# Performance work log

Measured on AMD Instinct MI355X. Metric: run time of the kernel, lower is better.

Reference implementation:

```python
import jax, jax.numpy as jnp
import numpy as np

GRID_MIN, GRID_MAX, GRID_SIZE = -4.0, 4.0, 12
BANDWIDTH = (GRID_MAX - GRID_MIN) / max(GRID_SIZE - 1, 1)  # 8/11


def setup_inputs() -> dict:
    key = jax.random.key(0)
    k1, k2, k3, k4 = jax.random.split(key, 4)
    B, I, O, G = 16384, 512, 512, GRID_SIZE
    x = jax.random.normal(k1, (B, I), dtype=jnp.float32)
    coeff = jax.random.normal(k2, (I, O, G), dtype=jnp.float32) * 0.05
    base_w = jax.random.normal(k3, (O, I), dtype=jnp.float32) * (1.0 / np.sqrt(I))
    base_b = jax.random.normal(k4, (O,), dtype=jnp.float32) * 0.01
    centers = jnp.linspace(GRID_MIN, GRID_MAX, G, dtype=jnp.float32)
    return {"x": x, "coeff": coeff, "base_w": base_w, "base_b": base_b, "centers": centers}


def reference(x, coeff, base_w, base_b, centers):
    # RBF basis: [B, I, G]
    diff = (x[..., None] - centers) / jnp.float32(BANDWIDTH)
    basis = jnp.exp(-0.5 * diff * diff)
    # spline contraction over in_dim and grid: [B, O]
    spline = jnp.einsum('big,iog->bo', basis, coeff)
    # residual base linear (torch Linear: x @ W^T + b)
    return spline + x @ base_w.T + base_b
```

## Files before the change

kernel.cpp:

```cpp
#include <hip/hip_runtime.h>
#include <hip/hip_bf16.h>


#define M_DIM 16384
#define N_DIM 512
#define I_DIM 512
#define KTOT  6656
#define NSTEP 104

typedef short short8 __attribute__((ext_vector_type(8)));
typedef float f32x16 __attribute__((ext_vector_type(16)));
typedef unsigned int u32x4 __attribute__((ext_vector_type(4)));

#define CVTPK(dst, lo, hi) \
  asm("v_cvt_pk_bf16_f32 %0, %1, %2" : "=v"(dst) : "v"(lo), "v"(hi))

__device__ __forceinline__ unsigned short f2bf(float f) {
  union { float f; unsigned int u; } c; c.f = f;
  unsigned int r = (c.u + 0x7FFFu + ((c.u >> 16) & 1)) >> 16;
  return (unsigned short)r;
}

__global__ __launch_bounds__(256) void prep_w(const float* __restrict__ coeff,
                                              const float* __restrict__ base_w,
                                              unsigned short* __restrict__ Wb2) {
  int t = blockIdx.x * 256 + threadIdx.x;
  int e0 = (t & 1) * 4;
  int go = t >> 1;
  int o  = go & 511;
  int g  = go >> 9;
  int k4 = g * 8 + e0;
  int ic = k4 / 832;
  int rem = k4 - ic * 832;
  int slot = rem >> 6;
  int ii = rem & 63;
  int i = ic * 64 + ii;
  float v0, v1, v2, v3;
  if (slot == 0) {
    const float4 bw = *(const float4*)(base_w + (size_t)o * I_DIM + i);
    v0 = bw.x; v1 = bw.y; v2 = bw.z; v3 = bw.w;
  } else {
    int gg = slot - 1;
    const float* cp = coeff + (size_t)i * (N_DIM * 12) + o * 12 + gg;
    v0 = cp[0]; v1 = cp[6144]; v2 = cp[2 * 6144]; v3 = cp[3 * 6144];
  }
  ushort4 s;
  s.x = f2bf(v0); s.y = f2bf(v1); s.z = f2bf(v2); s.w = f2bf(v3);
  *(ushort4*)(Wb2 + (size_t)go * 8 + e0) = s;
}

__global__ __launch_bounds__(512, 2) void kan_gemm(const float* __restrict__ x,
                                                   const unsigned short* __restrict__ Wb2,
                                                   const float* __restrict__ bias,
                                                   float* __restrict__ out) {
  __shared__ unsigned short Asw[2][8 * 128 * 8];
  __shared__ unsigned short Bsw[2][8 * 256 * 8];

  const int tid  = threadIdx.x;
  const int lane = tid & 63;
  const int wid  = tid >> 6;
  const int wm   = wid >> 2, wn = wid & 3;

  const int rb = blockIdx.x >> 1;
  const int cb = blockIdx.x & 1;
  const int M0 = rb * 128;
  const int N0 = cb * 256;

  const int arow = tid & 127;
  const int kgp  = tid >> 7;
  const float* xg = x + (size_t)(M0 + arow) * I_DIM + kgp * 16;
  const int aoff0 = ((kgp * 2) * 128 + arow) * 16;
  const int aoff1 = ((kgp * 2 + 1) * 128 + arow) * 16;

  const unsigned short* bsrc[4];
  int bdst[4];
#pragma unroll
  for (int q = 0; q < 4; ++q) {
    bsrc[q] = Wb2 + ((size_t)wid * 512 + N0 + q * 64 + lane) * 8;
    bdst[q] = (wid * 256 + q * 64) * 16;
  }

  const int l31 = lane & 31;
  const int aBase = ((lane >> 5) * 128 + wm * 64 + l31) * 16;
  const int bBase = ((lane >> 5) * 256 + wn * 64 + l31) * 16;

  f32x16 acc[2][2];
#pragma unroll
  for (int i = 0; i < 2; ++i)
#pragma unroll
    for (int j = 0; j < 2; ++j)
#pragma unroll
      for (int r = 0; r < 16; ++r) acc[i][j][r] = 0.f;

  float4 xq[4];
#pragma unroll
  for (int q = 0; q < 4; ++q) xq[q] = *(const float4*)(xg + q * 4);
  float bb[16], ff[16];
  int gslot = 0, gic = 0;

  auto emitA = [&](char* pA) {
    unsigned int w[8];
    if (gslot == 0) {
      float f[16];
#pragma unroll
      for (int q = 0; q < 4; ++q) {
        f[q*4+0] = xq[q].x; f[q*4+1] = xq[q].y; f[q*4+2] = xq[q].z; f[q*4+3] = xq[q].w;
      }
#pragma unroll
      for (int j = 0; j < 8; ++j) CVTPK(w[j], f[2*j], f[2*j+1]);
      *(u32x4*)(pA + aoff0) = (u32x4){w[0], w[1], w[2], w[3]};
      *(u32x4*)(pA + aoff1) = (u32x4){w[4], w[5], w[6], w[7]};
#pragma unroll
      for (int j = 0; j < 16; ++j) {
        float u = fmaf(f[j], 1.375f, 5.5f);
        bb[j] = exp2f(-0.72134752044448170f * u * u);
        ff[j] = exp2f(fmaf(u, 1.44269504088896340f, -0.72134752044448170f));
      }
      if (gic < 7) {
        const float* xn = xg + (gic + 1) * 64;
#pragma unroll
        for (int q = 0; q < 4; ++q) xq[q] = *(const float4*)(xn + q * 4);
        ++gic;
      }
    } else {
#pragma unroll
      for (int j = 0; j < 8; ++j) CVTPK(w[j], bb[2*j], bb[2*j+1]);
      *(u32x4*)(pA + aoff0) = (u32x4){w[0], w[1], w[2], w[3]};
      *(u32x4*)(pA + aoff1) = (u32x4){w[4], w[5], w[6], w[7]};
#pragma unroll
      for (int j = 0; j < 16; ++j) {
        bb[j] *= ff[j];
        ff[j] *= 0.36787944117144233f;
      }
    }
    gslot = (gslot == 12) ? 0 : gslot + 1;
  };

  emitA((char*)&Asw[0][0]);
#pragma unroll
  for (int q = 0; q < 4; ++q)
    __builtin_amdgcn_global_load_lds(
        (const __attribute__((address_space(1))) void*)(bsrc[q]),
        (__attribute__((address_space(3))) void*)((char*)&Bsw[0][0] + bdst[q]), 16, 0, 0);
  __syncthreads();

  int buf = 0;
  for (int ks = 0; ks < NSTEP; ++ks) {
    const int nxt = buf ^ 1;
    if (ks < NSTEP - 1) {
      const size_t ko = (size_t)(ks + 1) * 32768;
#pragma unroll
      for (int q = 0; q < 4; ++q)
        __builtin_amdgcn_global_load_lds(
            (const __attribute__((address_space(1))) void*)(bsrc[q] + ko),
            (__attribute__((address_space(3))) void*)((char*)&Bsw[nxt][0] + bdst[q]), 16, 0, 0);
      emitA((char*)&Asw[nxt][0]);
    }
    const char* pA = (const char*)&Asw[buf][0];
    const char* pB = (const char*)&Bsw[buf][0];
#pragma unroll
    for (int s = 0; s < 4; ++s) {
      const char* a = pA + aBase + s * 4096;
      const char* b = pB + bBase + s * 8192;
      short8 a0 = *(const short8*)(a);
      short8 a1 = *(const short8*)(a + 512);
      short8 b0 = *(const short8*)(b);
      short8 b1 = *(const short8*)(b + 512);
      acc[0][0] = __builtin_amdgcn_mfma_f32_32x32x16_bf16(a0, b0, acc[0][0], 0, 0, 0);
      acc[0][1] = __builtin_amdgcn_mfma_f32_32x32x16_bf16(a0, b1, acc[0][1], 0, 0, 0);
      acc[1][0] = __builtin_amdgcn_mfma_f32_32x32x16_bf16(a1, b0, acc[1][0], 0, 0, 0);
      acc[1][1] = __builtin_amdgcn_mfma_f32_32x32x16_bf16(a1, b1, acc[1][1], 0, 0, 0);
    }
    __syncthreads();
    buf = nxt;
  }

  float bv[2];
#pragma unroll
  for (int fn = 0; fn < 2; ++fn) bv[fn] = bias[N0 + wn * 64 + fn * 32 + l31];
  const int rbase = (lane >> 5) * 4;
#pragma unroll
  for (int fm = 0; fm < 2; ++fm) {
#pragma unroll
    for (int fn = 0; fn < 2; ++fn) {
      const size_t cix = (size_t)(N0 + wn * 64 + fn * 32 + l31);
#pragma unroll
      for (int r = 0; r < 16; ++r) {
        int row = M0 + wm * 64 + fm * 32 + (r & 3) + 8 * (r >> 2) + rbase;
        out[(size_t)row * N_DIM + cix] = acc[fm][fn][r] + bv[fn];
      }
    }
  }
}

extern "C" void kernel_launch(void* const* d_in, const int* in_sizes, int n_in,
                              void* d_out, int out_size, void* d_ws, size_t ws_size,
                              hipStream_t stream) {
  const float* x      = (const float*)d_in[0];
  const float* coeff  = (const float*)d_in[1];
  const float* base_w = (const float*)d_in[2];
  const float* base_b = (const float*)d_in[3];
  unsigned short* Wb2 = (unsigned short*)d_ws;

  prep_w<<<3328, 256, 0, stream>>>(coeff, base_w, Wb2);
  kan_gemm<<<256, 512, 0, stream>>>(x, Wb2, base_b, (float*)d_out);
}
```

Baseline: 138.0 us.

## Triple-buffer B tiles with prefetch distance two and manual waitcnt barriers

Grows the B shared-memory buffer from two to three stages and issues global-to-LDS loads two steps ahead. The full __syncthreads is replaced by explicit s_waitcnt vmcnt counts, so later loads can stay in flight across the barrier. It also raises wave priority around the MFMA block. This hides global load latency better, but uses more LDS, which may affect 2-blocks-per-CU occupancy, and the hand-tuned vmcnt counts are fragile.

```diff
diff --git a/kernel.cpp b/kernel.cpp
--- a/kernel.cpp
+++ b/kernel.cpp
@@ -54,7 +54,7 @@
                                                    const float* __restrict__ bias,
                                                    float* __restrict__ out) {
   __shared__ unsigned short Asw[2][8 * 128 * 8];
-  __shared__ unsigned short Bsw[2][8 * 256 * 8];
+  __shared__ unsigned short Bsw[3][8 * 256 * 8];
 
   const int tid  = threadIdx.x;
   const int lane = tid & 63;
@@ -96,83 +96,138 @@
 #pragma unroll
   for (int q = 0; q < 4; ++q) xq[q] = *(const float4*)(xg + q * 4);
   float bb[16], ff[16];
-  int gslot = 0, gic = 0;
-
-  auto emitA = [&](char* pA) {
-    unsigned int w[8];
-    if (gslot == 0) {
-      float f[16];
-#pragma unroll
-      for (int q = 0; q < 4; ++q) {
-        f[q*4+0] = xq[q].x; f[q*4+1] = xq[q].y; f[q*4+2] = xq[q].z; f[q*4+3] = xq[q].w;
-      }
-#pragma unroll
-      for (int j = 0; j < 8; ++j) CVTPK(w[j], f[2*j], f[2*j+1]);
-      *(u32x4*)(pA + aoff0) = (u32x4){w[0], w[1], w[2], w[3]};
-      *(u32x4*)(pA + aoff1) = (u32x4){w[4], w[5], w[6], w[7]};
-#pragma unroll
-      for (int j = 0; j < 16; ++j) {
-        float u = fmaf(f[j], 1.375f, 5.5f);
-        bb[j] = exp2f(-0.72134752044448170f * u * u);
-        ff[j] = exp2f(fmaf(u, 1.44269504088896340f, -0.72134752044448170f));
-      }
-      if (gic < 7) {
-        const float* xn = xg + (gic + 1) * 64;
-#pragma unroll
-        for (int q = 0; q < 4; ++q) xq[q] = *(const float4*)(xn + q * 4);
-        ++gic;
-      }
-    } else {
-#pragma unroll
-      for (int j = 0; j < 8; ++j) CVTPK(w[j], bb[2*j], bb[2*j+1]);
-      *(u32x4*)(pA + aoff0) = (u32x4){w[0], w[1], w[2], w[3]};
-      *(u32x4*)(pA + aoff1) = (u32x4){w[4], w[5], w[6], w[7]};
-#pragma unroll
-      for (int j = 0; j < 16; ++j) {
-        bb[j] *= ff[j];
-        ff[j] *= 0.36787944117144233f;
-      }
-    }
-    gslot = (gslot == 12) ? 0 : gslot + 1;
-  };
-
-  emitA((char*)&Asw[0][0]);
+  int gic = 0;
+
+  float f0[16];
+#pragma unroll
+  for (int q = 0; q < 4; ++q) {
+    f0[q*4+0] = xq[q].x; f0[q*4+1] = xq[q].y; f0[q*4+2] = xq[q].z; f0[q*4+3] = xq[q].w;
+  }
+#pragma unroll
+  for (int q = 0; q < 4; ++q) xq[q] = *(const float4*)(xg + 64 + q * 4);
+  gic = 1;
 #pragma unroll
   for (int q = 0; q < 4; ++q)
     __builtin_amdgcn_global_load_lds(
         (const __attribute__((address_space(1))) void*)(bsrc[q]),
         (__attribute__((address_space(3))) void*)((char*)&Bsw[0][0] + bdst[q]), 16, 0, 0);
-  __syncthreads();
-
-  int buf = 0;
-  for (int ks = 0; ks < NSTEP; ++ks) {
-    const int nxt = buf ^ 1;
-    if (ks < NSTEP - 1) {
-      const size_t ko = (size_t)(ks + 1) * 32768;
+#pragma unroll
+  for (int q = 0; q < 4; ++q)
+    __builtin_amdgcn_global_load_lds(
+        (const __attribute__((address_space(1))) void*)(bsrc[q] + 32768),
+        (__attribute__((address_space(3))) void*)((char*)&Bsw[1][0] + bdst[q]), 16, 0, 0);
+  {
+    unsigned int w[8];
+#pragma unroll
+    for (int j = 0; j < 8; ++j) CVTPK(w[j], f0[2*j], f0[2*j+1]);
+    char* pA = (char*)&Asw[0][0];
+    *(u32x4*)(pA + aoff0) = (u32x4){w[0], w[1], w[2], w[3]};
+    *(u32x4*)(pA + aoff1) = (u32x4){w[4], w[5], w[6], w[7]};
+#pragma unroll
+    for (int j = 0; j < 16; ++j) {
+      float u = fmaf(f0[j], 1.375f, 5.5f);
+      bb[j] = exp2f(-0.72134752044448170f * u * u);
+      ff[j] = exp2f(fmaf(u, 1.44269504088896340f, -0.72134752044448170f));
+    }
+  }
+  __builtin_amdgcn_sched_barrier(0);
+  asm volatile("s_waitcnt vmcnt(4) lgkmcnt(0)" ::: "memory");
+  __builtin_amdgcn_sched_barrier(0);
+  __builtin_amdgcn_s_barrier();
+  __builtin_amdgcn_sched_barrier(0);
+
+  int nslot = 1;
+  int cur3  = 0;
+  for (int t = 0; t < NSTEP; ++t) {
+    const bool emit = (t < NSTEP - 1);
+    const bool s0   = (nslot == 0);
+    bool reload = false;
+    float f[16];
+
+    if (emit && s0) {
+#pragma unroll
+      for (int q = 0; q < 4; ++q) {
+        f[q*4+0] = xq[q].x; f[q*4+1] = xq[q].y; f[q*4+2] = xq[q].z; f[q*4+3] = xq[q].w;
+      }
+      if (gic < 7) {
+        const float* xn = xg + (size_t)(gic + 1) * 64;
+#pragma unroll
+        for (int q = 0; q < 4; ++q) xq[q] = *(const float4*)(xn + q * 4);
+        reload = true;
+      }
+      ++gic;
+    }
+
+    if (t < NSTEP - 2) {
+      const int nx3 = (cur3 >= 1) ? cur3 - 1 : 2;
+      char* bb2 = (char*)&Bsw[nx3][0];
+      const size_t ko = (size_t)(t + 2) * 32768;
 #pragma unroll
       for (int q = 0; q < 4; ++q)
         __builtin_amdgcn_global_load_lds(
             (const __attribute__((address_space(1))) void*)(bsrc[q] + ko),
-            (__attribute__((address_space(3))) void*)((char*)&Bsw[nxt][0] + bdst[q]), 16, 0, 0);
-      emitA((char*)&Asw[nxt][0]);
-    }
-    const char* pA = (const char*)&Asw[buf][0];
-    const char* pB = (const char*)&Bsw[buf][0];
-#pragma unroll
-    for (int s = 0; s < 4; ++s) {
-      const char* a = pA + aBase + s * 4096;
-      const char* b = pB + bBase + s * 8192;
-      short8 a0 = *(const short8*)(a);
-      short8 a1 = *(const short8*)(a + 512);
-      short8 b0 = *(const short8*)(b);
-      short8 b1 = *(const short8*)(b + 512);
-      acc[0][0] = __builtin_amdgcn_mfma_f32_32x32x16_bf16(a0, b0, acc[0][0], 0, 0, 0);
-      acc[0][1] = __builtin_amdgcn_mfma_f32_32x32x16_bf16(a0, b1, acc[0][1], 0, 0, 0);
-      acc[1][0] = __builtin_amdgcn_mfma_f32_32x32x16_bf16(a1, b0, acc[1][0], 0, 0, 0);
-      acc[1][1] = __builtin_amdgcn_mfma_f32_32x32x16_bf16(a1, b1, acc[1][1], 0, 0, 0);
-    }
-    __syncthreads();
-    buf = nxt;
+            (__attribute__((address_space(3))) void*)(bb2 + bdst[q]), 16, 0, 0);
+    }
+
+    if (emit) {
+      char* pA = (char*)&Asw[(t + 1) & 1][0];
+      unsigned int w[8];
+      if (s0) {
+#pragma unroll
+        for (int j = 0; j < 8; ++j) CVTPK(w[j], f[2*j], f[2*j+1]);
+        *(u32x4*)(pA + aoff0) = (u32x4){w[0], w[1], w[2], w[3]};
+        *(u32x4*)(pA + aoff1) = (u32x4){w[4], w[5], w[6], w[7]};
+#pragma unroll
+        for (int j = 0; j < 16; ++j) {
+          float u = fmaf(f[j], 1.375f, 5.5f);
+          bb[j] = exp2f(-0.72134752044448170f * u * u);
+          ff[j] = exp2f(fmaf(u, 1.44269504088896340f, -0.72134752044448170f));
+        }
+      } else {
+#pragma unroll
+        for (int j = 0; j < 8; ++j) CVTPK(w[j], bb[2*j], bb[2*j+1]);
+        *(u32x4*)(pA + aoff0) = (u32x4){w[0], w[1], w[2], w[3]};
+        *(u32x4*)(pA + aoff1) = (u32x4){w[4], w[5], w[6], w[7]};
+#pragma unroll
+        for (int j = 0; j < 16; ++j) {
+          bb[j] *= ff[j];
+          ff[j] *= 0.36787944117144233f;
+        }
+      }
+    }
+
+    {
+      const char* pA = (const char*)&Asw[t & 1][0];
+      const char* pB = (const char*)&Bsw[cur3][0];
+      __builtin_amdgcn_s_setprio(1);
+#pragma unroll
+      for (int s = 0; s < 4; ++s) {
+        const char* a = pA + aBase + s * 4096;
+        const char* b = pB + bBase + s * 8192;
+        short8 a0 = *(const short8*)(a);
+        short8 a1 = *(const short8*)(a + 512);
+        short8 b0 = *(const short8*)(b);
+        short8 b1 = *(const short8*)(b + 512);
+        acc[0][0] = __builtin_amdgcn_mfma_f32_32x32x16_bf16(a0, b0, acc[0][0], 0, 0, 0);
+        acc[0][1] = __builtin_amdgcn_mfma_f32_32x32x16_bf16(a0, b1, acc[0][1], 0, 0, 0);
+        acc[1][0] = __builtin_amdgcn_mfma_f32_32x32x16_bf16(a1, b0, acc[1][0], 0, 0, 0);
+        acc[1][1] = __builtin_amdgcn_mfma_f32_32x32x16_bf16(a1, b1, acc[1][1], 0, 0, 0);
+      }
+      __builtin_amdgcn_s_setprio(0);
+    }
+
+    __builtin_amdgcn_sched_barrier(0);
+    if (reload) {
+      asm volatile("s_waitcnt vmcnt(8) lgkmcnt(0)" ::: "memory");
+    } else {
+      asm volatile("s_waitcnt vmcnt(4) lgkmcnt(0)" ::: "memory");
+    }
+    __builtin_amdgcn_sched_barrier(0);
+    __builtin_amdgcn_s_barrier();
+    __builtin_amdgcn_sched_barrier(0);
+
+    nslot = (nslot == 12) ? 0 : nslot + 1;
+    cur3  = (cur3 == 2) ? 0 : cur3 + 1;
   }
 
   float bv[2];
```

Measured after the change: 149.8 us. +8.5%, slower.

## Generate A fragments in registers and triple-buffer W through LDS

Applied to the files above, without the earlier changes.

The GEMM no longer stages the RBF basis in shared memory. Each wave computes its own A fragments directly in registers from x and feeds them to MFMA. Only W goes through LDS, now in a 3-stage ring with partial vmcnt waits, and high priority is set around the MFMA blocks. Blocks shrink to 256 threads with 128x128 tiles and 512 blocks. This removes the LDS writes and reads for A, but every wave recomputes the exponentials for its rows, so basis work is duplicated across the four N-blocks and register pressure rises from the 64-entry bb/ff arrays.

```diff
diff --git a/kernel.cpp b/kernel.cpp
--- a/kernel.cpp
+++ b/kernel.cpp
@@ -2,7 +2,6 @@
 #include <hip/hip_bf16.h>
 
 
-#define M_DIM 16384
 #define N_DIM 512
 #define I_DIM 512
 #define KTOT  6656
@@ -10,7 +9,8 @@
 
 typedef short short8 __attribute__((ext_vector_type(8)));
 typedef float f32x16 __attribute__((ext_vector_type(16)));
-typedef unsigned int u32x4 __attribute__((ext_vector_type(4)));
+
+union Frag { unsigned int w[4]; short8 s; };
 
 #define CVTPK(dst, lo, hi) \
   asm("v_cvt_pk_bf16_f32 %0, %1, %2" : "=v"(dst) : "v"(lo), "v"(hi))
@@ -49,41 +49,44 @@
   *(ushort4*)(Wb2 + (size_t)go * 8 + e0) = s;
 }
 
-__global__ __launch_bounds__(512, 2) void kan_gemm(const float* __restrict__ x,
+__global__ __launch_bounds__(256, 2) void kan_gemm(const float* __restrict__ x,
                                                    const unsigned short* __restrict__ Wb2,
                                                    const float* __restrict__ bias,
                                                    float* __restrict__ out) {
-  __shared__ unsigned short Asw[2][8 * 128 * 8];
-  __shared__ unsigned short Bsw[2][8 * 256 * 8];
+  __shared__ unsigned short Bsw[3 * 8 * 128 * 8];
 
   const int tid  = threadIdx.x;
   const int lane = tid & 63;
   const int wid  = tid >> 6;
-  const int wm   = wid >> 2, wn = wid & 3;
-
-  const int rb = blockIdx.x >> 1;
-  const int cb = blockIdx.x & 1;
-  const int M0 = rb * 128;
-  const int N0 = cb * 256;
-
-  const int arow = tid & 127;
-  const int kgp  = tid >> 7;
-  const float* xg = x + (size_t)(M0 + arow) * I_DIM + kgp * 16;
-  const int aoff0 = ((kgp * 2) * 128 + arow) * 16;
-  const int aoff1 = ((kgp * 2 + 1) * 128 + arow) * 16;
-
-  const unsigned short* bsrc[4];
-  int bdst[4];
-#pragma unroll
-  for (int q = 0; q < 4; ++q) {
-    bsrc[q] = Wb2 + ((size_t)wid * 512 + N0 + q * 64 + lane) * 8;
-    bdst[q] = (wid * 256 + q * 64) * 16;
-  }
-
-  const int l31 = lane & 31;
-  const int aBase = ((lane >> 5) * 128 + wm * 64 + l31) * 16;
-  const int bBase = ((lane >> 5) * 256 + wn * 64 + l31) * 16;
-
+  const int wb   = wid >> 1, wo = wid & 1;
+  const int l31  = lane & 31, h = lane >> 5;
+
+  const int M0 = (blockIdx.x >> 2) * 128;
+  const int N0 = (blockIdx.x & 3) * 128;
+
+  const unsigned short* wsrc[4];
+  int wdst[4];
+#pragma unroll
+  for (int r = 0; r < 4; ++r) {
+    int u  = r * 256 + tid;
+    int kg = u >> 7, o = u & 127;
+    wsrc[r] = Wb2 + ((size_t)kg * 512 + N0 + o) * 8;
+    wdst[r] = u * 8;
+  }
+
+#define STAGE(T_, RING_) do {                                                  \
+    const size_t ko_ = (size_t)(T_) * 32768;                                   \
+    unsigned short* d_ = Bsw + (RING_) * 8192;                                 \
+    _Pragma("unroll")                                                          \
+    for (int r_ = 0; r_ < 4; ++r_)                                             \
+      __builtin_amdgcn_global_load_lds(                                        \
+          (const __attribute__((address_space(1))) void*)(wsrc[r_] + ko_),     \
+          (__attribute__((address_space(3))) void*)(d_ + wdst[r_]), 16, 0, 0); \
+  } while (0)
+
+  const int rdB = (h * 128 + wo * 64 + l31) * 16;
+
+  float bb[2][32], ff[2][32];
   f32x16 acc[2][2];
 #pragma unroll
   for (int i = 0; i < 2; ++i)
@@ -92,102 +95,113 @@
 #pragma unroll
       for (int r = 0; r < 16; ++r) acc[i][j][r] = 0.f;
 
-  float4 xq[4];
-#pragma unroll
-  for (int q = 0; q < 4; ++q) xq[q] = *(const float4*)(xg + q * 4);
-  float bb[16], ff[16];
-  int gslot = 0, gic = 0;
-
-  auto emitA = [&](char* pA) {
-    unsigned int w[8];
-    if (gslot == 0) {
-      float f[16];
-#pragma unroll
-      for (int q = 0; q < 4; ++q) {
-        f[q*4+0] = xq[q].x; f[q*4+1] = xq[q].y; f[q*4+2] = xq[q].z; f[q*4+3] = xq[q].w;
-      }
-#pragma unroll
-      for (int j = 0; j < 8; ++j) CVTPK(w[j], f[2*j], f[2*j+1]);
-      *(u32x4*)(pA + aoff0) = (u32x4){w[0], w[1], w[2], w[3]};
-      *(u32x4*)(pA + aoff1) = (u32x4){w[4], w[5], w[6], w[7]};
-#pragma unroll
-      for (int j = 0; j < 16; ++j) {
-        float u = fmaf(f[j], 1.375f, 5.5f);
-        bb[j] = exp2f(-0.72134752044448170f * u * u);
-        ff[j] = exp2f(fmaf(u, 1.44269504088896340f, -0.72134752044448170f));
-      }
-      if (gic < 7) {
-        const float* xn = xg + (gic + 1) * 64;
-#pragma unroll
-        for (int q = 0; q < 4; ++q) xq[q] = *(const float4*)(xn + q * 4);
-        ++gic;
-      }
-    } else {
-#pragma unroll
-      for (int j = 0; j < 8; ++j) CVTPK(w[j], bb[2*j], bb[2*j+1]);
-      *(u32x4*)(pA + aoff0) = (u32x4){w[0], w[1], w[2], w[3]};
-      *(u32x4*)(pA + aoff1) = (u32x4){w[4], w[5], w[6], w[7]};
-#pragma unroll
-      for (int j = 0; j < 16; ++j) {
-        bb[j] *= ff[j];
-        ff[j] *= 0.36787944117144233f;
-      }
+  const float* xrow0 = x + (size_t)(M0 + wb * 64 + l31) * I_DIM + h * 8;
+  const float* xrow1 = xrow0 + (size_t)32 * I_DIM;
+
+  STAGE(0, 0);
+  STAGE(1, 1);
+  asm volatile("s_waitcnt vmcnt(4)" ::: "memory");
+  __builtin_amdgcn_s_barrier();
+
+  int t = 0, cur3 = 0;
+
+  for (int ic = 0; ic < 8; ++ic) {
+    {
+      Frag af[2][4];
+#pragma unroll
+      for (int fb = 0; fb < 2; ++fb) {
+        const float* xp = (fb ? xrow1 : xrow0) + ic * 64;
+#pragma unroll
+        for (int s = 0; s < 4; ++s) {
+          float4 p = *(const float4*)(xp + s * 16);
+          float4 q = *(const float4*)(xp + s * 16 + 4);
+          float f[8] = {p.x, p.y, p.z, p.w, q.x, q.y, q.z, q.w};
+#pragma unroll
+          for (int j2 = 0; j2 < 4; ++j2) CVTPK(af[fb][s].w[j2], f[2 * j2], f[2 * j2 + 1]);
+#pragma unroll
+          for (int e = 0; e < 8; ++e) {
+            float u = fmaf(f[e], 1.375f, 5.5f);
+            bb[fb][s * 8 + e] = exp2f(-0.72134752044448170f * u * u);
+            ff[fb][s * 8 + e] = exp2f(fmaf(u, 1.44269504088896340f, -0.72134752044448170f));
+          }
+        }
+      }
+      {
+        int nx = cur3 + 2; if (nx >= 3) nx -= 3;
+        if (t + 2 < NSTEP) STAGE(t + 2, nx);
+      }
+      const char* pB = (const char*)Bsw + cur3 * 16384;
+      __builtin_amdgcn_s_setprio(1);
+#pragma unroll
+      for (int s = 0; s < 4; ++s) {
+        short8 b0 = *(const short8*)(pB + rdB + s * 4096);
+        short8 b1 = *(const short8*)(pB + rdB + s * 4096 + 512);
+        acc[0][0] = __builtin_amdgcn_mfma_f32_32x32x16_bf16(af[0][s].s, b0, acc[0][0], 0, 0, 0);
+        acc[0][1] = __builtin_amdgcn_mfma_f32_32x32x16_bf16(af[0][s].s, b1, acc[0][1], 0, 0, 0);
+        acc[1][0] = __builtin_amdgcn_mfma_f32_32x32x16_bf16(af[1][s].s, b0, acc[1][0], 0, 0, 0);
+        acc[1][1] = __builtin_amdgcn_mfma_f32_32x32x16_bf16(af[1][s].s, b1, acc[1][1], 0, 0, 0);
+      }
+      __builtin_amdgcn_s_setprio(0);
+      asm volatile("s_waitcnt vmcnt(4) lgkmcnt(0)" ::: "memory");
+      __builtin_amdgcn_s_barrier();
+      ++t; cur3 = (cur3 == 2) ? 0 : cur3 + 1;
     }
-    gslot = (gslot == 12) ? 0 : gslot + 1;
-  };
-
-  emitA((char*)&Asw[0][0]);
-#pragma unroll
-  for (int q = 0; q < 4; ++q)
-    __builtin_amdgcn_global_load_lds(
-        (const __attribute__((address_space(1))) void*)(bsrc[q]),
-        (__attribute__((address_space(3))) void*)((char*)&Bsw[0][0] + bdst[q]), 16, 0, 0);
-  __syncthreads();
-
-  int buf = 0;
-  for (int ks = 0; ks < NSTEP; ++ks) {
-    const int nxt = buf ^ 1;
-    if (ks < NSTEP - 1) {
-      const size_t ko = (size_t)(ks + 1) * 32768;
-#pragma unroll
-      for (int q = 0; q < 4; ++q)
-        __builtin_amdgcn_global_load_lds(
-            (const __attribute__((address_space(1))) void*)(bsrc[q] + ko),
-            (__attribute__((address_space(3))) void*)((char*)&Bsw[nxt][0] + bdst[q]), 16, 0, 0);
-      emitA((char*)&Asw[nxt][0]);
+
+#pragma unroll 1
+    for (int s5 = 1; s5 < 13; ++s5) {
+      {
+        int nx = cur3 + 2; if (nx >= 3) nx -= 3;
+        if (t + 2 < NSTEP) STAGE(t + 2, nx);
+      }
+      Frag af[2][4];
+#pragma unroll
+      for (int fb = 0; fb < 2; ++fb)
+#pragma unroll
+        for (int s = 0; s < 4; ++s)
+#pragma unroll
+          for (int j2 = 0; j2 < 4; ++j2)
+            CVTPK(af[fb][s].w[j2], bb[fb][s * 8 + 2 * j2], bb[fb][s * 8 + 2 * j2 + 1]);
+
+      const char* pB = (const char*)Bsw + cur3 * 16384;
+      __builtin_amdgcn_s_setprio(1);
+#pragma unroll
+      for (int s = 0; s < 4; ++s) {
+        short8 b0 = *(const short8*)(pB + rdB + s * 4096);
+        short8 b1 = *(const short8*)(pB + rdB + s * 4096 + 512);
+        acc[0][0] = __builtin_amdgcn_mfma_f32_32x32x16_bf16(af[0][s].s, b0, acc[0][0], 0, 0, 0);
+        acc[0][1] = __builtin_amdgcn_mfma_f32_32x32x16_bf16(af[0][s].s, b1, acc[0][1], 0, 0, 0);
+        acc[1][0] = __builtin_amdgcn_mfma_f32_32x32x16_bf16(af[1][s].s, b0, acc[1][0], 0, 0, 0);
+        acc[1][1] = __builtin_amdgcn_mfma_f32_32x32x16_bf16(af[1][s].s, b1, acc[1][1], 0, 0, 0);
+      }
+      __builtin_amdgcn_s_setprio(0);
+
+#pragma unroll
+      for (int fb = 0; fb < 2; ++fb)
+#pragma unroll
+        for (int j = 0; j < 32; ++j) {
+          bb[fb][j] *= ff[fb][j];
+          ff[fb][j] *= 0.36787944117144233f;
+        }
+
+      asm volatile("s_waitcnt vmcnt(4) lgkmcnt(0)" ::: "memory");
+      __builtin_amdgcn_s_barrier();
+      ++t; cur3 = (cur3 == 2) ? 0 : cur3 + 1;
     }
-    const char* pA = (const char*)&Asw[buf][0];
-    const char* pB = (const char*)&Bsw[buf][0];
-#pragma unroll
-    for (int s = 0; s < 4; ++s) {
-      const char* a = pA + aBase + s * 4096;
-      const char* b = pB + bBase + s * 8192;
-      short8 a0 = *(const short8*)(a);
-      short8 a1 = *(const short8*)(a + 512);
-      short8 b0 = *(const short8*)(b);
-      short8 b1 = *(const short8*)(b + 512);
-      acc[0][0] = __builtin_amdgcn_mfma_f32_32x32x16_bf16(a0, b0, acc[0][0], 0, 0, 0);
-      acc[0][1] = __builtin_amdgcn_mfma_f32_32x32x16_bf16(a0, b1, acc[0][1], 0, 0, 0);
-      acc[1][0] = __builtin_amdgcn_mfma_f32_32x32x16_bf16(a1, b0, acc[1][0], 0, 0, 0);
-      acc[1][1] = __builtin_amdgcn_mfma_f32_32x32x16_bf16(a1, b1, acc[1][1], 0, 0, 0);
-    }
-    __syncthreads();
-    buf = nxt;
   }
 
   float bv[2];
 #pragma unroll
-  for (int fn = 0; fn < 2; ++fn) bv[fn] = bias[N0 + wn * 64 + fn * 32 + l31];
-  const int rbase = (lane >> 5) * 4;
-#pragma unroll
-  for (int fm = 0; fm < 2; ++fm) {
-#pragma unroll
-    for (int fn = 0; fn < 2; ++fn) {
-      const size_t cix = (size_t)(N0 + wn * 64 + fn * 32 + l31);
+  for (int fo = 0; fo < 2; ++fo) bv[fo] = bias[N0 + wo * 64 + fo * 32 + l31];
+  const int rbase = 4 * h;
+#pragma unroll
+  for (int fb = 0; fb < 2; ++fb) {
+#pragma unroll
+    for (int fo = 0; fo < 2; ++fo) {
+      const size_t cix = (size_t)(N0 + wo * 64 + fo * 32 + l31);
 #pragma unroll
       for (int r = 0; r < 16; ++r) {
-        int row = M0 + wm * 64 + fm * 32 + (r & 3) + 8 * (r >> 2) + rbase;
-        out[(size_t)row * N_DIM + cix] = acc[fm][fn][r] + bv[fn];
+        int row = M0 + wb * 64 + fb * 32 + (r & 3) + 8 * (r >> 2) + rbase;
+        out[(size_t)row * N_DIM + cix] = acc[fb][fo][r] + bv[fo];
       }
     }
   }
@@ -203,5 +217,5 @@
   unsigned short* Wb2 = (unsigned short*)d_ws;
 
   prep_w<<<3328, 256, 0, stream>>>(coeff, base_w, Wb2);
-  kan_gemm<<<256, 512, 0, stream>>>(x, Wb2, base_b, (float*)d_out);
-}
+  kan_gemm<<<512, 256, 0, stream>>>(x, Wb2, base_b, (float*)d_out);
+}
```

Result: slower. 198.9 us (+44.1%).

## Shrink GEMM tile to 128x128 with 4 waves and XCD-aware block mapping

Applied to the files above, without the earlier changes.

The fused KAN GEMM moves from 512-thread blocks on 128x256 tiles to 256-thread blocks on 128x128 tiles, which doubles the grid to 512 blocks. Each thread now builds 32 basis values per row segment instead of 16. Block IDs are remapped so that blocks on the same XCD share a column block, to improve L2 reuse of the weight tile. The x prefetch register pipeline is removed, so x is now loaded synchronously inside emitA. This halves B reuse per block and doubles the per-thread RBF work and register pressure, which may hurt occupancy.

```diff
diff --git a/kernel.cpp b/kernel.cpp
--- a/kernel.cpp
+++ b/kernel.cpp
@@ -2,7 +2,6 @@
 #include <hip/hip_bf16.h>
 
 
-#define M_DIM 16384
 #define N_DIM 512
 #define I_DIM 512
 #define KTOT  6656
@@ -49,40 +48,55 @@
   *(ushort4*)(Wb2 + (size_t)go * 8 + e0) = s;
 }
 
-__global__ __launch_bounds__(512, 2) void kan_gemm(const float* __restrict__ x,
+__global__ __launch_bounds__(256, 2) void kan_gemm(const float* __restrict__ x,
                                                    const unsigned short* __restrict__ Wb2,
                                                    const float* __restrict__ bias,
                                                    float* __restrict__ out) {
   __shared__ unsigned short Asw[2][8 * 128 * 8];
-  __shared__ unsigned short Bsw[2][8 * 256 * 8];
+  __shared__ unsigned short Bsw[2][8 * 128 * 8];
 
   const int tid  = threadIdx.x;
   const int lane = tid & 63;
   const int wid  = tid >> 6;
-  const int wm   = wid >> 2, wn = wid & 3;
-
-  const int rb = blockIdx.x >> 1;
-  const int cb = blockIdx.x & 1;
-  const int M0 = rb * 128;
-  const int N0 = cb * 256;
+  const int rowg = wid >> 1, colg = wid & 1;
+  const int l31  = lane & 31, hl = lane >> 5;
+
+  const int bid = blockIdx.x;
+  const int xcd = bid & 7, jj = bid >> 3;
+  const int cb  = xcd >> 1;
+  const int rb  = (xcd & 1) * 64 + jj;
+  const int M0  = rb * 128;
+  const int N0  = cb * 128;
 
   const int arow = tid & 127;
   const int kgp  = tid >> 7;
-  const float* xg = x + (size_t)(M0 + arow) * I_DIM + kgp * 16;
-  const int aoff0 = ((kgp * 2) * 128 + arow) * 16;
-  const int aoff1 = ((kgp * 2 + 1) * 128 + arow) * 16;
-
-  const unsigned short* bsrc[4];
-  int bdst[4];
-#pragma unroll
-  for (int q = 0; q < 4; ++q) {
-    bsrc[q] = Wb2 + ((size_t)wid * 512 + N0 + q * 64 + lane) * 8;
-    bdst[q] = (wid * 256 + q * 64) * 16;
-  }
-
-  const int l31 = lane & 31;
-  const int aBase = ((lane >> 5) * 128 + wm * 64 + l31) * 16;
-  const int bBase = ((lane >> 5) * 256 + wn * 64 + l31) * 16;
+  const float* xg = x + (size_t)(M0 + arow) * I_DIM + kgp * 32;
+  int aoff[4];
+#pragma unroll
+  for (int q = 0; q < 4; ++q) aoff[q] = ((kgp * 4 + q) * 128 + arow) * 16;
+
+  const unsigned short* wsrc[4];
+  int wdst[4];
+#pragma unroll
+  for (int r = 0; r < 4; ++r) {
+    int u  = r * 256 + tid;
+    int kg = u >> 7, col = u & 127;
+    wsrc[r] = Wb2 + ((size_t)kg * 512 + N0 + col) * 8;
+    wdst[r] = u * 8;
+  }
+
+#define STAGE(T_, BUF_) do {                                                   \
+    const size_t ko_ = (size_t)(T_) * 32768;                                   \
+    unsigned short* d_ = &Bsw[BUF_][0];                                        \
+    _Pragma("unroll")                                                          \
+    for (int r_ = 0; r_ < 4; ++r_)                                             \
+      __builtin_amdgcn_global_load_lds(                                        \
+          (const __attribute__((address_space(1))) void*)(wsrc[r_] + ko_),     \
+          (__attribute__((address_space(3))) void*)(d_ + wdst[r_]), 16, 0, 0); \
+  } while (0)
+
+  const int aBase = (hl * 128 + rowg * 64 + l31) * 16;
+  const int bBase = (hl * 128 + colg * 64 + l31) * 16;
 
   f32x16 acc[2][2];
 #pragma unroll
@@ -92,43 +106,39 @@
 #pragma unroll
       for (int r = 0; r < 16; ++r) acc[i][j][r] = 0.f;
 
-  float4 xq[4];
-#pragma unroll
-  for (int q = 0; q < 4; ++q) xq[q] = *(const float4*)(xg + q * 4);
-  float bb[16], ff[16];
+  float bb[32], ff[32];
   int gslot = 0, gic = 0;
 
   auto emitA = [&](char* pA) {
-    unsigned int w[8];
+    unsigned int w[16];
     if (gslot == 0) {
-      float f[16];
-#pragma unroll
-      for (int q = 0; q < 4; ++q) {
-        f[q*4+0] = xq[q].x; f[q*4+1] = xq[q].y; f[q*4+2] = xq[q].z; f[q*4+3] = xq[q].w;
-      }
-#pragma unroll
-      for (int j = 0; j < 8; ++j) CVTPK(w[j], f[2*j], f[2*j+1]);
-      *(u32x4*)(pA + aoff0) = (u32x4){w[0], w[1], w[2], w[3]};
-      *(u32x4*)(pA + aoff1) = (u32x4){w[4], w[5], w[6], w[7]};
-#pragma unroll
-      for (int j = 0; j < 16; ++j) {
+      float f[32];
+      const float* xp = xg + (size_t)gic * 64;
+#pragma unroll
+      for (int q = 0; q < 8; ++q) {
+        float4 p = *(const float4*)(xp + q * 4);
+        f[q*4+0] = p.x; f[q*4+1] = p.y; f[q*4+2] = p.z; f[q*4+3] = p.w;
+      }
+#pragma unroll
+      for (int j = 0; j < 16; ++j) CVTPK(w[j], f[2*j], f[2*j+1]);
+#pragma unroll
+      for (int q = 0; q < 4; ++q)
+        *(u32x4*)(pA + aoff[q]) = (u32x4){w[q*4], w[q*4+1], w[q*4+2], w[q*4+3]};
+#pragma unroll
+      for (int j = 0; j < 32; ++j) {
         float u = fmaf(f[j], 1.375f, 5.5f);
         bb[j] = exp2f(-0.72134752044448170f * u * u);
         ff[j] = exp2f(fmaf(u, 1.44269504088896340f, -0.72134752044448170f));
       }
-      if (gic < 7) {
-        const float* xn = xg + (gic + 1) * 64;
-#pragma unroll
-        for (int q = 0; q < 4; ++q) xq[q] = *(const float4*)(xn + q * 4);
-        ++gic;
-      }
+      ++gic;
     } else {
 #pragma unroll
-      for (int j = 0; j < 8; ++j) CVTPK(w[j], bb[2*j], bb[2*j+1]);
-      *(u32x4*)(pA + aoff0) = (u32x4){w[0], w[1], w[2], w[3]};
-      *(u32x4*)(pA + aoff1) = (u32x4){w[4], w[5], w[6], w[7]};
-#pragma unroll
-      for (int j = 0; j < 16; ++j) {
+      for (int j = 0; j < 16; ++j) CVTPK(w[j], bb[2*j], bb[2*j+1]);
+#pragma unroll
+      for (int q = 0; q < 4; ++q)
+        *(u32x4*)(pA + aoff[q]) = (u32x4){w[q*4], w[q*4+1], w[q*4+2], w[q*4+3]};
+#pragma unroll
+      for (int j = 0; j < 32; ++j) {
         bb[j] *= ff[j];
         ff[j] *= 0.36787944117144233f;
       }
@@ -137,57 +147,44 @@
   };
 
   emitA((char*)&Asw[0][0]);
-#pragma unroll
-  for (int q = 0; q < 4; ++q)
-    __builtin_amdgcn_global_load_lds(
-        (const __attribute__((address_space(1))) void*)(bsrc[q]),
-        (__attribute__((address_space(3))) void*)((char*)&Bsw[0][0] + bdst[q]), 16, 0, 0);
+  STAGE(0, 0);
   __syncthreads();
 
-  int buf = 0;
-  for (int ks = 0; ks < NSTEP; ++ks) {
-    const int nxt = buf ^ 1;
-    if (ks < NSTEP - 1) {
-      const size_t ko = (size_t)(ks + 1) * 32768;
-#pragma unroll
-      for (int q = 0; q < 4; ++q)
-        __builtin_amdgcn_global_load_lds(
-            (const __attribute__((address_space(1))) void*)(bsrc[q] + ko),
-            (__attribute__((address_space(3))) void*)((char*)&Bsw[nxt][0] + bdst[q]), 16, 0, 0);
+  for (int t = 0; t < NSTEP; ++t) {
+    const int buf = t & 1, nxt = buf ^ 1;
+    if (t < NSTEP - 1) {
+      STAGE(t + 1, nxt);
       emitA((char*)&Asw[nxt][0]);
     }
     const char* pA = (const char*)&Asw[buf][0];
     const char* pB = (const char*)&Bsw[buf][0];
 #pragma unroll
     for (int s = 0; s < 4; ++s) {
-      const char* a = pA + aBase + s * 4096;
-      const char* b = pB + bBase + s * 8192;
-      short8 a0 = *(const short8*)(a);
-      short8 a1 = *(const short8*)(a + 512);
-      short8 b0 = *(const short8*)(b);
-      short8 b1 = *(const short8*)(b + 512);
+      short8 a0 = *(const short8*)(pA + aBase + s * 4096);
+      short8 a1 = *(const short8*)(pA + aBase + s * 4096 + 512);
+      short8 b0 = *(const short8*)(pB + bBase + s * 4096);
+      short8 b1 = *(const short8*)(pB + bBase + s * 4096 + 512);
       acc[0][0] = __builtin_amdgcn_mfma_f32_32x32x16_bf16(a0, b0, acc[0][0], 0, 0, 0);
       acc[0][1] = __builtin_amdgcn_mfma_f32_32x32x16_bf16(a0, b1, acc[0][1], 0, 0, 0);
       acc[1][0] = __builtin_amdgcn_mfma_f32_32x32x16_bf16(a1, b0, acc[1][0], 0, 0, 0);
       acc[1][1] = __builtin_amdgcn_mfma_f32_32x32x16_bf16(a1, b1, acc[1][1], 0, 0, 0);
     }
     __syncthreads();
-    buf = nxt;
   }
 
   float bv[2];
 #pragma unroll
-  for (int fn = 0; fn < 2; ++fn) bv[fn] = bias[N0 + wn * 64 + fn * 32 + l31];
-  const int rbase = (lane >> 5) * 4;
-#pragma unroll
-  for (int fm = 0; fm < 2; ++fm) {
-#pragma unroll
-    for (int fn = 0; fn < 2; ++fn) {
-      const size_t cix = (size_t)(N0 + wn * 64 + fn * 32 + l31);
+  for (int fo = 0; fo < 2; ++fo) bv[fo] = bias[N0 + colg * 64 + fo * 32 + l31];
+  const int rbase = 4 * hl;
+#pragma unroll
+  for (int fb = 0; fb < 2; ++fb) {
+#pragma unroll
+    for (int fo = 0; fo < 2; ++fo) {
+      const size_t cix = (size_t)(N0 + colg * 64 + fo * 32 + l31);
 #pragma unroll
       for (int r = 0; r < 16; ++r) {
-        int row = M0 + wm * 64 + fm * 32 + (r & 3) + 8 * (r >> 2) + rbase;
-        out[(size_t)row * N_DIM + cix] = acc[fm][fn][r] + bv[fn];
+        int row = M0 + rowg * 64 + fb * 32 + (r & 3) + 8 * (r >> 2) + rbase;
+        out[(size_t)row * N_DIM + cix] = acc[fb][fo][r] + bv[fo];
       }
     }
   }
@@ -203,5 +200,5 @@
   unsigned short* Wb2 = (unsigned short*)d_ws;
 
   prep_w<<<3328, 256, 0, stream>>>(coeff, base_w, Wb2);
-  kan_gemm<<<256, 512, 0, stream>>>(x, Wb2, base_b, (float*)d_out);
-}
+  kan_gemm<<<512, 256, 0, stream>>>(x, Wb2, base_b, (float*)d_out);
+}
```

After: 145.1 us. +5.1%, slower.
